# Kernel optimization log

Hardware: AMD Instinct MI355X
Metric: run time of the kernel (lower is better)

The kernel has to match this reference:

```python
import jax, jax.numpy as jnp
import numpy as np

S, B, C = 56, 5, 20
N = 128


def _cxcywh_to_xyxy(b):
    cx, cy, w, h = b[..., 0], b[..., 1], b[..., 2], b[..., 3]
    return jnp.stack([cx - 0.5 * w, cy - 0.5 * h, cx + 0.5 * w, cy + 0.5 * h], axis=-1)


def setup_inputs() -> dict:
    key = jax.random.key(0)
    k1, k2, k3 = jax.random.split(key, 3)
    predicts_tensor = jax.random.normal(k1, (N, S, S, B, C + 5), dtype=jnp.float32)
    targets_tensor = jax.random.uniform(k2, (N, S, S, C + 5), dtype=jnp.float32)
    anchors = jax.random.uniform(k3, (B, 2), dtype=jnp.float32)
    return {"predicts_tensor": predicts_tensor, "targets_tensor": targets_tensor, "anchors": anchors}


def reference(predicts_tensor, targets_tensor, anchors):
    p = predicts_tensor.reshape(-1, S, S, B, C + 5)
    # decode: sigmoid on cx,cy ; exp * anchor on w,h
    xy = jax.nn.sigmoid(p[..., C + 1:C + 3])
    wh = jnp.exp(p[..., C + 3:]) * anchors  # anchors [B,2] broadcasts over [...,B,2]
    p = jnp.concatenate([p[..., :C + 1], xy, wh], axis=-1)

    pb = _cxcywh_to_xyxy(p[..., C + 1:])                         # [N,S,S,B,4]
    tb = _cxcywh_to_xyxy(targets_tensor[..., C + 1:])[..., None, :]  # [N,S,S,1,4]

    # torchvision box_iou, vectorized over all cells and B boxes
    lt = jnp.maximum(pb[..., :2], tb[..., :2])
    rb = jnp.minimum(pb[..., 2:], tb[..., 2:])
    whi = jnp.clip(rb - lt, 0.0)
    inter = whi[..., 0] * whi[..., 1]
    area_p = (pb[..., 2] - pb[..., 0]) * (pb[..., 3] - pb[..., 1])
    area_t = (tb[..., 2] - tb[..., 0]) * (tb[..., 3] - tb[..., 1])
    ious = inter / (area_p + area_t - inter)                     # [N,S,S,B]

    best_idx = jnp.argmax(ious, axis=-1)                         # [N,S,S]
    pbest = jnp.take_along_axis(p, best_idx[..., None, None], axis=3)[..., 0, :]  # [N,S,S,C+5]
    pbest = pbest.at[..., 0].set(pbest[..., 0] * best_idx.astype(pbest.dtype))

    exists = targets_tensor[..., C:C + 1]
    sse = lambda a, b: jnp.sum((a - b) ** 2)  # MSELoss(reduction='sum')

    loss_xcyc = sse(exists * pbest[..., C + 1:C + 3], exists * targets_tensor[..., C + 1:C + 3])
    p_wh = pbest[..., C + 3:]
    p_wh = jnp.sign(p_wh) * jnp.sqrt(jnp.abs(p_wh) + 1e-6)
    loss_wh = sse(exists * p_wh, exists * targets_tensor[..., C + 3:])
    loss_cls = sse(exists * pbest[..., :C], exists * targets_tensor[..., :C])
    loss_obj = sse(exists * pbest[..., C:C + 1], exists * targets_tensor[..., C:C + 1])
    noobj = 1.0 - exists
    loss_noobj = sse(noobj * pbest[..., C:C + 1], noobj * targets_tensor[..., C:C + 1])

    return loss_xcyc + loss_wh + loss_cls + loss_noobj + loss_obj
```

## Files before the change

### kernel.cpp

```cpp
#include <hip/hip_runtime.h>

constexpr int S_   = 56;
constexpr int B_   = 5;
constexpr int C_   = 20;
constexpr int N_   = 128;
constexpr int CELLS = N_ * S_ * S_;
constexpr int PSTR  = B_ * (C_ + 5);
constexpr int TSTR  = C_ + 5;

constexpr int TPB  = 256;
constexpr int NBLK = CELLS / TPB;

constexpr int NBUCKET       = 64;
constexpr int BUCKET_STRIDE = 32;

__global__ __launch_bounds__(TPB, 4) void yolo_loss_kernel(
    const float* __restrict__ pred,
    const float* __restrict__ targ,
    const float* __restrict__ anch,
    float* __restrict__ buckets)
{
    const int cell = blockIdx.x * TPB + threadIdx.x;
    const float* __restrict__ pc = pred + (size_t)cell * PSTR;
    const float* __restrict__ tp = targ + (size_t)cell * TSTR;

    float t[TSTR];
    #pragma unroll
    for (int k = 0; k < TSTR; ++k) t[k] = tp[k];

    float pobj[B_], prx[B_], pry[B_], prw[B_], prh[B_];
    #pragma unroll
    for (int b = 0; b < B_; ++b) {
        pobj[b] = pc[b * TSTR + C_];
        prx[b]  = pc[b * TSTR + C_ + 1];
        pry[b]  = pc[b * TSTR + C_ + 2];
        prw[b]  = pc[b * TSTR + C_ + 3];
        prh[b]  = pc[b * TSTR + C_ + 4];
    }

    float aw[B_], ah[B_];
    #pragma unroll
    for (int b = 0; b < B_; ++b) { aw[b] = anch[2 * b]; ah[b] = anch[2 * b + 1]; }

    const float tcx = t[C_ + 1], tcy = t[C_ + 2];
    const float tw  = t[C_ + 3], th  = t[C_ + 4];
    const float tx0 = tcx - 0.5f * tw, ty0 = tcy - 0.5f * th;
    const float tx1 = tcx + 0.5f * tw, ty1 = tcy + 0.5f * th;
    const float area_t = tw * th;

    float best_iou = -1.f;
    int   best_b = 0;
    float bcx = 0.f, bcy = 0.f, bw = 0.f, bh = 0.f, bobj = 0.f;

    #pragma unroll
    for (int b = 0; b < B_; ++b) {
        const float cx = __builtin_amdgcn_rcpf(1.f + __expf(-prx[b]));
        const float cy = __builtin_amdgcn_rcpf(1.f + __expf(-pry[b]));
        const float w  = __expf(prw[b]) * aw[b];
        const float h  = __expf(prh[b]) * ah[b];

        const float x0 = cx - 0.5f * w, y0 = cy - 0.5f * h;
        const float x1 = cx + 0.5f * w, y1 = cy + 0.5f * h;

        float wi = fminf(x1, tx1) - fmaxf(x0, tx0);
        float hi = fminf(y1, ty1) - fmaxf(y0, ty0);
        wi = fmaxf(wi, 0.f);
        hi = fmaxf(hi, 0.f);
        const float inter = wi * hi;
        const float iou = inter * __builtin_amdgcn_rcpf(w * h + area_t - inter);

        const bool better = iou > best_iou;
        best_iou = better ? iou : best_iou;
        best_b   = better ? b   : best_b;
        bcx  = better ? cx      : bcx;
        bcy  = better ? cy      : bcy;
        bw   = better ? w       : bw;
        bh   = better ? h       : bh;
        bobj = better ? pobj[b] : bobj;
    }

    const float* pb = pc + best_b * TSTR;
    float acc = 0.f;
    #pragma unroll
    for (int k = 0; k < C_; ++k) {
        float v = pb[k];
        if (k == 0) v *= (float)best_b;
        const float d = v - t[k];
        acc = fmaf(d, d, acc);
    }

    float d;
    d = bcx - tcx; acc = fmaf(d, d, acc);
    d = bcy - tcy; acc = fmaf(d, d, acc);

    d = sqrtf(bw + 1e-6f) - tw; acc = fmaf(d, d, acc);
    d = sqrtf(bh + 1e-6f) - th; acc = fmaf(d, d, acc);

    const float e    = t[C_];
    const float ne   = 1.f - e;
    const float dobj = bobj - e;
    float local = e * e * acc + (e * e + ne * ne) * (dobj * dobj);

    #pragma unroll
    for (int off = 32; off > 0; off >>= 1)
        local += __shfl_down(local, off, 64);

    if ((threadIdx.x & 63) == 0) {
        const int wid = (blockIdx.x << 2) | (threadIdx.x >> 6);
        atomicAdd(&buckets[(wid & (NBUCKET - 1)) * BUCKET_STRIDE], local);
    }
}

__global__ __launch_bounds__(64) void finalize_kernel(
    const float* __restrict__ buckets, float* __restrict__ out)
{
    float v = buckets[threadIdx.x * BUCKET_STRIDE];
    #pragma unroll
    for (int off = 32; off > 0; off >>= 1)
        v += __shfl_down(v, off, 64);
    if (threadIdx.x == 0) out[0] = v;
}

extern "C" void kernel_launch(void* const* d_in, const int* in_sizes, int n_in,
                              void* d_out, int out_size, void* d_ws, size_t ws_size,
                              hipStream_t stream) {
    const float* pred = (const float*)d_in[0];
    const float* targ = (const float*)d_in[1];
    const float* anch = (const float*)d_in[2];
    float* out     = (float*)d_out;
    float* buckets = (float*)d_ws;

    hipMemsetAsync(buckets, 0, NBUCKET * BUCKET_STRIDE * sizeof(float), stream);

    yolo_loss_kernel<<<NBLK, TPB, 0, stream>>>(pred, targ, anch, buckets);
    finalize_kernel<<<1, 64, 0, stream>>>(buckets, out);
}
```

Baseline: 320.2 us.

## Stage prediction rows into LDS via async global_load_lds and drop atomics

```diff
diff --git a/kernel.cpp b/kernel.cpp
--- a/kernel.cpp
+++ b/kernel.cpp
@@ -8,35 +8,40 @@
 constexpr int PSTR  = B_ * (C_ + 5);
 constexpr int TSTR  = C_ + 5;
 
-constexpr int TPB  = 256;
-constexpr int NBLK = CELLS / TPB;
+constexpr int CPB    = 64;
+constexpr int NBLK   = CELLS / CPB;
+constexpr int PRED_B = CPB * PSTR * 4;
 
-constexpr int NBUCKET       = 64;
-constexpr int BUCKET_STRIDE = 32;
+__device__ __forceinline__ void gload_lds16(const char* g, char* l) {
+    __builtin_amdgcn_global_load_lds(
+        (const __attribute__((address_space(1))) void*)g,
+        (__attribute__((address_space(3))) void*)l,
+        16, 0, 0);
+}
 
-__global__ __launch_bounds__(TPB, 4) void yolo_loss_kernel(
+__global__ __launch_bounds__(64) void yolo_loss_kernel(
     const float* __restrict__ pred,
     const float* __restrict__ targ,
     const float* __restrict__ anch,
-    float* __restrict__ buckets)
+    float* __restrict__ part)
 {
-    const int cell = blockIdx.x * TPB + threadIdx.x;
-    const float* __restrict__ pc = pred + (size_t)cell * PSTR;
+    __shared__ char lds[PRED_B];
+
+    const int lane  = threadIdx.x;
+    const int cell0 = blockIdx.x * CPB;
+    const int cell  = cell0 + lane;
+
+    const char* gp = (const char*)(pred + (size_t)cell0 * PSTR);
+    #pragma unroll
+    for (int it = 0; it < 31; ++it)
+        gload_lds16(gp + it * 1024 + lane * 16, lds + it * 1024);
+    if (lane < 16)
+        gload_lds16(gp + 31744 + lane * 16, lds + 31744);
+
     const float* __restrict__ tp = targ + (size_t)cell * TSTR;
-
     float t[TSTR];
     #pragma unroll
     for (int k = 0; k < TSTR; ++k) t[k] = tp[k];
-
-    float pobj[B_], prx[B_], pry[B_], prw[B_], prh[B_];
-    #pragma unroll
-    for (int b = 0; b < B_; ++b) {
-        pobj[b] = pc[b * TSTR + C_];
-        prx[b]  = pc[b * TSTR + C_ + 1];
-        pry[b]  = pc[b * TSTR + C_ + 2];
-        prw[b]  = pc[b * TSTR + C_ + 3];
-        prh[b]  = pc[b * TSTR + C_ + 4];
-    }
 
     float aw[B_], ah[B_];
     #pragma unroll
@@ -48,16 +53,25 @@
     const float tx1 = tcx + 0.5f * tw, ty1 = tcy + 0.5f * th;
     const float area_t = tw * th;
 
+    __syncthreads();
+
+    const float* pc = (const float*)lds + (size_t)lane * PSTR;
+
     float best_iou = -1.f;
     int   best_b = 0;
-    float bcx = 0.f, bcy = 0.f, bw = 0.f, bh = 0.f, bobj = 0.f;
+    float bcx = 0.f, bcy = 0.f, bw = 0.f, bh = 0.f;
 
     #pragma unroll
     for (int b = 0; b < B_; ++b) {
-        const float cx = __builtin_amdgcn_rcpf(1.f + __expf(-prx[b]));
-        const float cy = __builtin_amdgcn_rcpf(1.f + __expf(-pry[b]));
-        const float w  = __expf(prw[b]) * aw[b];
-        const float h  = __expf(prh[b]) * ah[b];
+        const float rcx = pc[b * TSTR + C_ + 1];
+        const float rcy = pc[b * TSTR + C_ + 2];
+        const float rw  = pc[b * TSTR + C_ + 3];
+        const float rh  = pc[b * TSTR + C_ + 4];
+
+        const float cx = __builtin_amdgcn_rcpf(1.f + __expf(-rcx));
+        const float cy = __builtin_amdgcn_rcpf(1.f + __expf(-rcy));
+        const float w  = __expf(rw) * aw[b];
+        const float h  = __expf(rh) * ah[b];
 
         const float x0 = cx - 0.5f * w, y0 = cy - 0.5f * h;
         const float x1 = cx + 0.5f * w, y1 = cy + 0.5f * h;
@@ -72,14 +86,14 @@
         const bool better = iou > best_iou;
         best_iou = better ? iou : best_iou;
         best_b   = better ? b   : best_b;
-        bcx  = better ? cx      : bcx;
-        bcy  = better ? cy      : bcy;
-        bw   = better ? w       : bw;
-        bh   = better ? h       : bh;
-        bobj = better ? pobj[b] : bobj;
+        bcx = better ? cx : bcx;
+        bcy = better ? cy : bcy;
+        bw  = better ? w  : bw;
+        bh  = better ? h  : bh;
     }
 
     const float* pb = pc + best_b * TSTR;
+
     float acc = 0.f;
     #pragma unroll
     for (int k = 0; k < C_; ++k) {
@@ -98,27 +112,38 @@
 
     const float e    = t[C_];
     const float ne   = 1.f - e;
-    const float dobj = bobj - e;
+    const float dobj = pb[C_] - e;
     float local = e * e * acc + (e * e + ne * ne) * (dobj * dobj);
 
     #pragma unroll
     for (int off = 32; off > 0; off >>= 1)
         local += __shfl_down(local, off, 64);
 
-    if ((threadIdx.x & 63) == 0) {
-        const int wid = (blockIdx.x << 2) | (threadIdx.x >> 6);
-        atomicAdd(&buckets[(wid & (NBUCKET - 1)) * BUCKET_STRIDE], local);
-    }
+    if (lane == 0)
+        part[blockIdx.x] = local;
 }
 
-__global__ __launch_bounds__(64) void finalize_kernel(
-    const float* __restrict__ buckets, float* __restrict__ out)
+__global__ __launch_bounds__(1024) void finalize_kernel(
+    const float* __restrict__ part, float* __restrict__ out)
 {
-    float v = buckets[threadIdx.x * BUCKET_STRIDE];
+    float v = 0.f;
+    for (int i = threadIdx.x; i < NBLK; i += 1024)
+        v += part[i];
+
     #pragma unroll
     for (int off = 32; off > 0; off >>= 1)
         v += __shfl_down(v, off, 64);
-    if (threadIdx.x == 0) out[0] = v;
+
+    __shared__ float ws[16];
+    if ((threadIdx.x & 63) == 0) ws[threadIdx.x >> 6] = v;
+    __syncthreads();
+    if (threadIdx.x < 16) {
+        float x = ws[threadIdx.x];
+        #pragma unroll
+        for (int off = 8; off > 0; off >>= 1)
+            x += __shfl_down(x, off, 16);
+        if (threadIdx.x == 0) out[0] = x;
+    }
 }
 
 extern "C" void kernel_launch(void* const* d_in, const int* in_sizes, int n_in,
@@ -127,11 +152,9 @@
     const float* pred = (const float*)d_in[0];
     const float* targ = (const float*)d_in[1];
     const float* anch = (const float*)d_in[2];
-    float* out     = (float*)d_out;
-    float* buckets = (float*)d_ws;
+    float* out  = (float*)d_out;
+    float* part = (float*)d_ws;
 
-    hipMemsetAsync(buckets, 0, NBUCKET * BUCKET_STRIDE * sizeof(float), stream);
-
-    yolo_loss_kernel<<<NBLK, TPB, 0, stream>>>(pred, targ, anch, buckets);
-    finalize_kernel<<<1, 64, 0, stream>>>(buckets, out);
+    yolo_loss_kernel<<<NBLK, CPB, 0, stream>>>(pred, targ, anch, part);
+    finalize_kernel<<<1, 1024, 0, stream>>>(part, out);
 }
```

Result: faster. 305.6 us (-4.6%).
